# Performance work log

Measured on AMD Instinct MI355X. Metric: run time of the kernel, lower is better.

Reference implementation:

```python
import jax, jax.numpy as jnp
import numpy as np

# BQQ block dims: Y_sign (p,j,k,m,l), Z_sign (p,j,k,l,n); in=k*n=4096, out=j*m=4096
P, J, K, M, L, N = 2, 32, 32, 128, 16, 128
ACT_BITS = 8  # activation quantization bits


def setup_inputs() -> dict:
    key = jax.random.key(0)
    ks = jax.random.split(key, 7)
    x = jax.random.normal(ks[0], (1, 512, K * N), dtype=jnp.float32)
    # sign matrices in {-1,+1}
    Y_sign = jnp.where(jax.random.normal(ks[1], (P, J, K, M, L)) >= 0, 1.0, -1.0).astype(jnp.float32)
    Z_sign = jnp.where(jax.random.normal(ks[2], (P, J, K, L, N)) >= 0, 1.0, -1.0).astype(jnp.float32)
    # per-block positive scales (abs-mean in the original, so strictly > 0)
    Y_scale = jax.random.uniform(ks[3], (P, J, K, 1, 1), minval=0.01, maxval=0.1, dtype=jnp.float32)
    Z_scale = jax.random.uniform(ks[4], (P, J, K, 1, 1), minval=0.01, maxval=0.1, dtype=jnp.float32)
    A = jax.random.normal(ks[5], (P, J, K, 4), dtype=jnp.float32) * 0.1
    bias = jax.random.normal(ks[6], (J * M,), dtype=jnp.float32) * 0.1
    return {"input": x, "Y_sign": Y_sign, "Z_sign": Z_sign,
            "Y_scale": Y_scale, "Z_scale": Z_scale, "A": A, "bias": bias}


def reference(input, Y_sign, Z_sign, Y_scale, Z_scale, A, bias):
    # --- activation quantization (act_bits = 8, simple round, no STE) ---
    qmax = float(2 ** (ACT_BITS - 1) - 1)  # 127
    x_max = jnp.max(input)
    x_min = jnp.min(input)
    act_scale = jnp.maximum((x_max - x_min) / (2.0 * qmax), 1e-8)
    X = jnp.clip(jnp.round(input / act_scale), -qmax, qmax) * act_scale

    # --- dequantize sign * scale ---
    Y_q = Y_sign * Y_scale  # (p,j,k,m,l)
    Z_q = Z_sign * Z_scale  # (p,j,k,l,n)

    orig_shape = X.shape[:-1]
    X_kn = X.reshape(-1, K, N)  # (B,k,n)

    # chained block einsums
    T = jnp.einsum('bkn,pjkln->bpjkl', X_kn, Z_q)          # (B,p,j,k,l)
    core = jnp.einsum('pjkml,bpjkl->bpjkm', Y_q, T)        # (B,p,j,k,m)

    # quant_bias=True correction terms: A[...,0..3] = (a,b,c,d)
    out1 = jnp.einsum('bpjkm,pjk->bjm', core, A[..., 0])

    Y_sum = Y_q.sum(axis=-1)                               # (p,j,k,m)
    B_coef = jnp.einsum('pjk,pjkm->jkm', A[..., 1], Y_sum)
    Sx = X_kn.sum(axis=-1)                                 # (B,k)
    out2 = jnp.einsum('bk,jkm->bjm', Sx, B_coef)

    Zs = Z_q.sum(axis=-2)                                  # (p,j,k,n)
    Tz = jnp.einsum('bkn,pjkn->bpjk', X_kn, Zs)
    out3 = jnp.einsum('bpjk,pjk->bj', Tz, A[..., 2])

    D_coef = A[..., 3].sum(axis=0)                         # (j,k)
    out4 = jnp.einsum('bk,jk->bj', Sx, D_coef)

    out_bjm = out1 + out2 + (out3 + out4)[:, :, None]      # (B,j,m)
    out_2d = out_bjm.reshape(-1, J * M) + bias
    return out_2d.reshape(*orig_shape, J * M)
```

## Files before the change

### kernel.cpp

```cpp
#include <hip/hip_runtime.h>
#include <hip/hip_bf16.h>

typedef __attribute__((ext_vector_type(4))) float f32x4;
typedef __attribute__((ext_vector_type(8))) short bf16x8;
typedef __attribute__((ext_vector_type(4))) unsigned int u32x4;

#define GLOBAL_AS __attribute__((address_space(1)))
#define LDS_AS __attribute__((address_space(3)))

static __device__ __forceinline__ unsigned short f2bf(float f) {
  __hip_bfloat16 h = __float2bfloat16(f);
  return __builtin_bit_cast(unsigned short, h);
}
static __device__ __forceinline__ float bf2f(unsigned short u) {
  unsigned int v = ((unsigned int)u) << 16;
  return __builtin_bit_cast(float, v);
}
static __device__ __forceinline__ void load_lds16(const void* g, void* l) {
  __builtin_amdgcn_global_load_lds((GLOBAL_AS void*)g, (LDS_AS void*)l, 16, 0, 0);
}

__global__ __launch_bounds__(256) void k_minmax_part(const float* __restrict__ x,
                                                     float* __restrict__ part) {
  int tid = blockIdx.x * 256 + threadIdx.x;
  const float4* xv = (const float4*)x;
  float mn = 3.4e38f, mx = -3.4e38f;
#pragma unroll
  for (int rep = 0; rep < 8; ++rep) {
    float4 v = xv[tid + rep * 65536];
    mn = fminf(mn, fminf(fminf(v.x, v.y), fminf(v.z, v.w)));
    mx = fmaxf(mx, fmaxf(fmaxf(v.x, v.y), fmaxf(v.z, v.w)));
  }
#pragma unroll
  for (int o = 32; o > 0; o >>= 1) {
    mn = fminf(mn, __shfl_down(mn, o));
    mx = fmaxf(mx, __shfl_down(mx, o));
  }
  __shared__ float smn[4], smx[4];
  int lane = threadIdx.x & 63, w = threadIdx.x >> 6;
  if (lane == 0) { smn[w] = mn; smx[w] = mx; }
  __syncthreads();
  if (threadIdx.x == 0) {
    mn = fminf(fminf(smn[0], smn[1]), fminf(smn[2], smn[3]));
    mx = fmaxf(fmaxf(smx[0], smx[1]), fmaxf(smx[2], smx[3]));
    part[2 * blockIdx.x] = mn;
    part[2 * blockIdx.x + 1] = mx;
  }
}

__global__ __launch_bounds__(256) void k_fused(const float* __restrict__ x,
                                               const float* __restrict__ part,
                                               const float* __restrict__ Ysg,
                                               const float* __restrict__ Zsg,
                                               const float* __restrict__ Ysc,
                                               const float* __restrict__ Zsc,
                                               const float* __restrict__ Acoef,
                                               float* __restrict__ scl,
                                               unsigned short* __restrict__ xq,
                                               unsigned short* __restrict__ W) {
  const int t = threadIdx.x;
  if (blockIdx.x < 1024) {
    const int jk = blockIdx.x;
    __shared__ unsigned short Yb[2 * 128 * 24];
    __shared__ unsigned short Zb[128 * 36];
    __shared__ float B1p[2][128];
    __shared__ float C1[128];
    float cf0[2], cf2[2], cf4[2];
    float Dv;
    {
      float ys0 = Ysc[jk], zs0 = Zsc[jk], ys1 = Ysc[1024 + jk], zs1 = Zsc[1024 + jk];
      const float* A0p = Acoef + (size_t)jk * 4;
      const float* A1p = Acoef + (size_t)(1024 + jk) * 4;
      cf0[0] = A0p[0] * ys0 * zs0; cf0[1] = A1p[0] * ys1 * zs1;
      cf2[0] = A0p[1] * ys0;       cf2[1] = A1p[1] * ys1;
      cf4[0] = A0p[2] * zs0;       cf4[1] = A1p[2] * zs1;
      Dv = A0p[3] + A1p[3];
    }
#pragma unroll
    for (int rep = 0; rep < 4; ++rep) {
      int q = rep * 256 + t;
      int l0 = (q & 3) * 4, m = (q >> 2) & 127, p = q >> 9;
      float4 v = *(const float4*)(Ysg + (size_t)(p * 1024 + jk) * 2048 + m * 16 + l0);
      float s4 = v.x + v.y + v.z + v.w;
      s4 += __shfl_xor(s4, 1);
      s4 += __shfl_xor(s4, 2);
      if ((t & 3) == 0) B1p[p][m] = s4;
      float c0 = cf0[p];
      ushort4 o = make_ushort4(f2bf(c0 * v.x), f2bf(c0 * v.y), f2bf(c0 * v.z), f2bf(c0 * v.w));
      *(ushort4*)&Yb[(p * 128 + m) * 24 + l0] = o;
    }
#pragma unroll
    for (int rep = 0; rep < 4; ++rep) {
      int q = rep * 256 + t;
      int n0 = (q & 31) * 4, l = (q >> 5) & 15, p = q >> 9;
      float4 v = *(const float4*)(Zsg + (size_t)(p * 1024 + jk) * 2048 + l * 128 + n0);
      int pl = p * 16 + l;
      Zb[(n0 + 0) * 36 + pl] = f2bf(v.x);
      Zb[(n0 + 1) * 36 + pl] = f2bf(v.y);
      Zb[(n0 + 2) * 36 + pl] = f2bf(v.z);
      Zb[(n0 + 3) * 36 + pl] = f2bf(v.w);
    }
    __syncthreads();
    if (t < 128) {
      float s0 = 0.f, s1 = 0.f;
#pragma unroll
      for (int l = 0; l < 16; ++l) {
        s0 += bf2f(Zb[t * 36 + l]);
        s1 += bf2f(Zb[t * 36 + 16 + l]);
      }
      C1[t] = cf4[0] * s0 + cf4[1] * s1;
    }
    __syncthreads();
    const int lane = t & 63, wid = t >> 6;
    const int wm = wid >> 1, wn = wid & 1;
    const int grp = lane >> 4;
    bf16x8 af[4], bfr[4];
#pragma unroll
    for (int fm = 0; fm < 4; ++fm) {
      int m = wm * 64 + fm * 16 + (lane & 15);
      af[fm] = *(const bf16x8*)((const char*)Yb + ((grp >> 1) * 128 + m) * 48 + (grp & 1) * 16);
    }
#pragma unroll
    for (int fn = 0; fn < 4; ++fn) {
      int n = wn * 64 + fn * 16 + (lane & 15);
      const char* zp = (const char*)Zb + n * 72 + grp * 16;
      uint2 z0 = *(const uint2*)zp;
      uint2 z1 = *(const uint2*)(zp + 8);
      u32x4 zw; zw[0] = z0.x; zw[1] = z0.y; zw[2] = z1.x; zw[3] = z1.y;
      bfr[fn] = __builtin_bit_cast(bf16x8, zw);
    }
    f32x4 acc[4][4];
#pragma unroll
    for (int fm = 0; fm < 4; ++fm)
#pragma unroll
      for (int fn = 0; fn < 4; ++fn)
        acc[fm][fn] = __builtin_amdgcn_mfma_f32_16x16x32_bf16(af[fm], bfr[fn], (f32x4)(0.f), 0, 0, 0);
    const int j = jk >> 5, k = jk & 31;
    float c1v[4];
#pragma unroll
    for (int fn = 0; fn < 4; ++fn) c1v[fn] = C1[wn * 64 + fn * 16 + (lane & 15)];
#pragma unroll
    for (int fm = 0; fm < 4; ++fm) {
#pragma unroll
      for (int i = 0; i < 4; ++i) {
        int row = wm * 64 + fm * 16 + (grp)*4 + i;
        float b1v = cf2[0] * B1p[0][row] + cf2[1] * B1p[1][row] + Dv;
        size_t rowoff = (size_t)(j * 128 + row) * 4096 + (size_t)(k * 128);
#pragma unroll
        for (int fn = 0; fn < 4; ++fn) {
          int col = wn * 64 + fn * 16 + (lane & 15);
          W[rowoff + col] = f2bf(acc[fm][fn][i] + b1v + c1v[fn]);
        }
      }
    }
  } else {
    const int qb = blockIdx.x - 1024;
    float2 v2 = ((const float2*)part)[t];
    float mn = v2.x, mx = v2.y;
#pragma unroll
    for (int o = 32; o > 0; o >>= 1) {
      mn = fminf(mn, __shfl_down(mn, o));
      mx = fmaxf(mx, __shfl_down(mx, o));
    }
    __shared__ float smn2[4], smx2[4], ssc[1];
    int lane = t & 63, w = t >> 6;
    if (lane == 0) { smn2[w] = mn; smx2[w] = mx; }
    __syncthreads();
    if (t == 0) {
      mn = fminf(fminf(smn2[0], smn2[1]), fminf(smn2[2], smn2[3]));
      mx = fmaxf(fmaxf(smx2[0], smx2[1]), fmaxf(smx2[2], smx2[3]));
      ssc[0] = fmaxf((mx - mn) / 254.0f, 1e-8f);
      if (qb == 0) scl[0] = ssc[0];
    }
    __syncthreads();
    const float s = ssc[0];
    int i = qb * 256 + t;
    float4 v = ((const float4*)x)[i];
    float a = fminf(fmaxf(rintf(v.x / s), -127.f), 127.f);
    float b = fminf(fmaxf(rintf(v.y / s), -127.f), 127.f);
    float c = fminf(fmaxf(rintf(v.z / s), -127.f), 127.f);
    float d = fminf(fmaxf(rintf(v.w / s), -127.f), 127.f);
    ((ushort4*)xq)[i] = make_ushort4(f2bf(a), f2bf(b), f2bf(c), f2bf(d));
  }
}

__global__ __launch_bounds__(512) void k_gemm(const unsigned short* __restrict__ Xq,
                                              const unsigned short* __restrict__ W,
                                              unsigned short* __restrict__ P) {
  __shared__ unsigned short Al[2][256 * 64];
  __shared__ unsigned short Bl[2][256 * 64];
  const int t = threadIdx.x, lane = t & 63, wid = t >> 6;
  const int wg = (blockIdx.x & 7) * 32 + (blockIdx.x >> 3);
  const int sk = wg >> 5;
  const int bm = (wg >> 4) & 1;
  const int bn = wg & 15;
  const int wm = wid >> 2, wn = wid & 3;
  const int kbase = sk * 512;
  f32x4 acc[8][4];
#pragma unroll
  for (int a = 0; a < 8; ++a)
#pragma unroll
    for (int b = 0; b < 4; ++b) acc[a][b] = (f32x4)(0.f);

  const int lr = lane >> 3;
  const int lcb = (lane & 7) * 16;

  auto STAGE = [&](int buf, int kt) {
    const int k0 = kbase + kt * 64;
#pragma unroll
    for (int c = 0; c < 4; ++c) {
      int chunk = wid * 4 + c;
      int r = chunk * 8 + lr;
      int colb = lcb ^ ((r & 7) << 4);
      load_lds16(Xq + ((size_t)(bm * 256 + r) << 12) + k0 + (colb >> 1), &Al[buf][chunk * 512]);
    }
#pragma unroll
    for (int c = 0; c < 4; ++c) {
      int chunk = wid * 4 + c;
      int r = chunk * 8 + lr;
      int colb = lcb ^ ((r & 7) << 4);
      load_lds16(W + ((size_t)(bn * 256 + r) << 12) + k0 + (colb >> 1), &Bl[buf][chunk * 512]);
    }
  };

  auto COMPUTE = [&](int buf) {
#pragma unroll
    for (int ks = 0; ks < 2; ++ks) {
      bf16x8 af[8], bfr[4];
#pragma unroll
      for (int fm = 0; fm < 8; ++fm) {
        int r = wm * 128 + fm * 16 + (lane & 15);
        int colb = (ks * 64 + ((lane >> 4) * 16)) ^ ((r & 7) << 4);
        af[fm] = *(const bf16x8*)((const char*)&Al[buf][0] + r * 128 + colb);
      }
#pragma unroll
      for (int fn = 0; fn < 4; ++fn) {
        int r = wn * 64 + fn * 16 + (lane & 15);
        int colb = (ks * 64 + ((lane >> 4) * 16)) ^ ((r & 7) << 4);
        bfr[fn] = *(const bf16x8*)((const char*)&Bl[buf][0] + r * 128 + colb);
      }
#pragma unroll
      for (int fm = 0; fm < 8; ++fm)
#pragma unroll
        for (int fn = 0; fn < 4; ++fn)
          acc[fm][fn] = __builtin_amdgcn_mfma_f32_16x16x32_bf16(af[fm], bfr[fn], acc[fm][fn], 0, 0, 0);
    }
  };

  STAGE(0, 0);
  for (int it = 0; it < 8; ++it) {
    STAGE((it + 1) & 1, (it + 1) & 7);
    __builtin_amdgcn_sched_barrier(0);
    asm volatile("s_waitcnt vmcnt(8)" ::: "memory");
    __builtin_amdgcn_sched_barrier(0);
    __builtin_amdgcn_s_barrier();
    __builtin_amdgcn_sched_barrier(0);
    COMPUTE(it & 1);
    __builtin_amdgcn_sched_barrier(0);
    __builtin_amdgcn_s_barrier();
  }

  unsigned short* Pk = P + (size_t)sk * 2097152;
  const int blkL = bm * 16 + bn;
#pragma unroll
  for (int fm = 0; fm < 8; ++fm) {
#pragma unroll
    for (int fn = 0; fn < 4; ++fn) {
      int idx = (((blkL * 8 + wid) * 32 + fm * 4 + fn) * 64) + lane;
      ushort4 o = make_ushort4(f2bf(acc[fm][fn][0]), f2bf(acc[fm][fn][1]),
                               f2bf(acc[fm][fn][2]), f2bf(acc[fm][fn][3]));
      ((ushort4*)Pk)[idx] = o;
    }
  }
}

__global__ __launch_bounds__(256) void k_epi(float* __restrict__ out,
                                             const unsigned short* __restrict__ P,
                                             const float* __restrict__ scl,
                                             const float* __restrict__ bias) {
  int g = blockIdx.x * 256 + threadIdx.x;
  const int lane = g & 63;
  const int ff = (g >> 6) & 31;
  const int fn = ff & 3, fm = ff >> 2;
  const int wid = (g >> 11) & 7;
  const int blkL = g >> 14;
  const int bm = blkL >> 4, bn = blkL & 15;
  const int wm = wid >> 2, wn = wid & 3;
  const int row0 = bm * 256 + wm * 128 + fm * 16 + ((lane >> 4) << 2);
  const int col = bn * 256 + wn * 64 + fn * 16 + (lane & 15);
  const float s = scl[0];
  const float bv = bias[col];
  float sum[4] = {0.f, 0.f, 0.f, 0.f};
#pragma unroll
  for (int k = 0; k < 8; ++k) {
    ushort4 p = ((const ushort4*)(P + (size_t)k * 2097152))[g];
    sum[0] += bf2f(p.x); sum[1] += bf2f(p.y); sum[2] += bf2f(p.z); sum[3] += bf2f(p.w);
  }
#pragma unroll
  for (int i = 0; i < 4; ++i) out[(size_t)(row0 + i) * 4096 + col] = sum[i] * s + bv;
}

__global__ __launch_bounds__(512) void k_gemm_fb(const unsigned short* __restrict__ Xq,
                                                 const unsigned short* __restrict__ W,
                                                 const float* __restrict__ scl,
                                                 const float* __restrict__ bias,
                                                 float* __restrict__ out) {
  __shared__ unsigned short Al[4][128 * 64];
  __shared__ unsigned short Bl[4][64 * 64];
  const int t = threadIdx.x, lane = t & 63, wid = t >> 6;
  const int wg = (blockIdx.x & 7) * 32 + (blockIdx.x >> 3);
  const int bm = wg & 3;
  const int bn = wg >> 2;
  const int wm = wid >> 1, wn = wid & 1;
  f32x4 acc[2][2];
#pragma unroll
  for (int a = 0; a < 2; ++a)
#pragma unroll
    for (int b = 0; b < 2; ++b) acc[a][b] = (f32x4)(0.f);
  const int lr = lane >> 3;
  const int lcb = (lane & 7) * 16;
  auto STAGE = [&](int buf, int kt) {
    const int k0 = kt * 64;
#pragma unroll
    for (int c = 0; c < 2; ++c) {
      int chunk = wid * 2 + c;
      int r = chunk * 8 + lr;
      int colb = lcb ^ ((r & 7) << 4);
      load_lds16(Xq + ((size_t)(bm * 128 + r) << 12) + k0 + (colb >> 1), &Al[buf][chunk * 512]);
    }
    {
      int r = wid * 8 + lr;
      int colb = lcb ^ ((r & 7) << 4);
      load_lds16(W + ((size_t)(bn * 64 + r) << 12) + k0 + (colb >> 1), &Bl[buf][wid * 512]);
    }
  };
  auto COMPUTE = [&](int buf) {
#pragma unroll
    for (int ks = 0; ks < 2; ++ks) {
      bf16x8 af[2], bfr[2];
#pragma unroll
      for (int fm = 0; fm < 2; ++fm) {
        int r = wm * 32 + fm * 16 + (lane & 15);
        int colb = (ks * 64 + ((lane >> 4) * 16)) ^ ((r & 7) << 4);
        af[fm] = *(const bf16x8*)((const char*)&Al[buf][0] + r * 128 + colb);
      }
#pragma unroll
      for (int fn = 0; fn < 2; ++fn) {
        int r = wn * 32 + fn * 16 + (lane & 15);
        int colb = (ks * 64 + ((lane >> 4) * 16)) ^ ((r & 7) << 4);
        bfr[fn] = *(const bf16x8*)((const char*)&Bl[buf][0] + r * 128 + colb);
      }
#pragma unroll
      for (int fm = 0; fm < 2; ++fm)
#pragma unroll
        for (int fn = 0; fn < 2; ++fn)
          acc[fm][fn] = __builtin_amdgcn_mfma_f32_16x16x32_bf16(af[fm], bfr[fn], acc[fm][fn], 0, 0, 0);
    }
  };
  STAGE(0, 0); STAGE(1, 1); STAGE(2, 2);
  for (int t64 = 0; t64 < 64; ++t64) {
    STAGE((t64 + 3) & 3, (t64 + 3) & 63);
    __builtin_amdgcn_sched_barrier(0);
    asm volatile("s_waitcnt vmcnt(9)" ::: "memory");
    __builtin_amdgcn_sched_barrier(0);
    __builtin_amdgcn_s_barrier();
    __builtin_amdgcn_sched_barrier(0);
    COMPUTE(t64 & 3);
    __builtin_amdgcn_sched_barrier(0);
    __builtin_amdgcn_s_barrier();
  }
  const float s = scl[0];
#pragma unroll
  for (int fn = 0; fn < 2; ++fn) {
    int col = bn * 64 + wn * 32 + fn * 16 + (lane & 15);
    float bv = bias[col];
#pragma unroll
    for (int fm = 0; fm < 2; ++fm) {
#pragma unroll
      for (int i = 0; i < 4; ++i) {
        int row = bm * 128 + wm * 32 + fm * 16 + (lane >> 4) * 4 + i;
        out[(size_t)row * 4096 + col] = acc[fm][fn][i] * s + bv;
      }
    }
  }
}

extern "C" void kernel_launch(void* const* d_in, const int* in_sizes, int n_in,
                              void* d_out, int out_size, void* d_ws, size_t ws_size,
                              hipStream_t stream) {
  const float* x    = (const float*)d_in[0];
  const float* Ysg  = (const float*)d_in[1];
  const float* Zsg  = (const float*)d_in[2];
  const float* Ysc  = (const float*)d_in[3];
  const float* Zsc  = (const float*)d_in[4];
  const float* A    = (const float*)d_in[5];
  const float* bias = (const float*)d_in[6];
  float* out = (float*)d_out;

  char* ws = (char*)d_ws;
  float* scl  = (float*)ws;
  float* part = (float*)(ws + 256);
  unsigned short* Xq = (unsigned short*)(ws + 65536);
  unsigned short* W  = (unsigned short*)(ws + 65536 + (size_t)4194304);
  unsigned short* P  = (unsigned short*)(ws + 65536 + (size_t)4194304 + (size_t)33554432);

  k_minmax_part<<<dim3(256), dim3(256), 0, stream>>>(x, part);
  k_fused<<<dim3(3072), dim3(256), 0, stream>>>(x, part, Ysg, Zsg, Ysc, Zsc, A, scl, Xq, W);
  if (ws_size >= (size_t)65536 + 4194304 + 33554432 + 33554432) {
    k_gemm<<<dim3(256), dim3(512), 0, stream>>>(Xq, W, P);
    k_epi<<<dim3(2048), dim3(256), 0, stream>>>(out, P, scl, bias);
  } else {
    k_gemm_fb<<<dim3(256), dim3(512), 0, stream>>>(Xq, W, scl, bias, out);
  }
}
```

Measured before the change: 55.55 us.

## Deepen GEMM LDS pipeline to four stages with 32-wide K tiles

The GEMM kernel's LDS staging moves from two 64-wide K buffers to four 32-wide K buffers, with three stages prefetched ahead and a matching vmcnt wait. The XOR swizzle is replaced by a rotation swizzle suited to 64-byte rows. MFMA issue is wrapped in s_setprio to favour the math wave during compute. The aim is to hide global-load latency better at the same LDS footprint, at the cost of twice as many barrier pairs per K and smaller compute chunks between syncs.

```diff
diff --git a/kernel.cpp b/kernel.cpp
--- a/kernel.cpp
+++ b/kernel.cpp
@@ -187,8 +187,8 @@
 __global__ __launch_bounds__(512) void k_gemm(const unsigned short* __restrict__ Xq,
                                               const unsigned short* __restrict__ W,
                                               unsigned short* __restrict__ P) {
-  __shared__ unsigned short Al[2][256 * 64];
-  __shared__ unsigned short Bl[2][256 * 64];
+  __shared__ unsigned short Al[4][256 * 32];
+  __shared__ unsigned short Bl[4][256 * 32];
   const int t = threadIdx.x, lane = t & 63, wid = t >> 6;
   const int wg = (blockIdx.x & 7) * 32 + (blockIdx.x >> 3);
   const int sk = wg >> 5;
@@ -202,60 +202,59 @@
 #pragma unroll
     for (int b = 0; b < 4; ++b) acc[a][b] = (f32x4)(0.f);
 
-  const int lr = lane >> 3;
-  const int lcb = (lane & 7) * 16;
+  const int srow = lane >> 2;
+  const int sphys = lane & 3;
 
   auto STAGE = [&](int buf, int kt) {
-    const int k0 = kbase + kt * 64;
-#pragma unroll
-    for (int c = 0; c < 4; ++c) {
-      int chunk = wid * 4 + c;
-      int r = chunk * 8 + lr;
-      int colb = lcb ^ ((r & 7) << 4);
-      load_lds16(Xq + ((size_t)(bm * 256 + r) << 12) + k0 + (colb >> 1), &Al[buf][chunk * 512]);
-    }
-#pragma unroll
-    for (int c = 0; c < 4; ++c) {
-      int chunk = wid * 4 + c;
-      int r = chunk * 8 + lr;
-      int colb = lcb ^ ((r & 7) << 4);
-      load_lds16(W + ((size_t)(bn * 256 + r) << 12) + k0 + (colb >> 1), &Bl[buf][chunk * 512]);
+    const int k0 = kbase + kt * 32;
+#pragma unroll
+    for (int c2 = 0; c2 < 2; ++c2) {
+      int chunk = wid * 2 + c2;
+      int r = chunk * 16 + srow;
+      int g = (sphys - (r >> 1)) & 3;
+      load_lds16(Xq + ((size_t)(bm * 256 + r) << 12) + k0 + g * 8, &Al[buf][chunk * 512]);
+    }
+#pragma unroll
+    for (int c2 = 0; c2 < 2; ++c2) {
+      int chunk = wid * 2 + c2;
+      int r = chunk * 16 + srow;
+      int g = (sphys - (r >> 1)) & 3;
+      load_lds16(W + ((size_t)(bn * 256 + r) << 12) + k0 + g * 8, &Bl[buf][chunk * 512]);
     }
   };
 
-  auto COMPUTE = [&](int buf) {
-#pragma unroll
-    for (int ks = 0; ks < 2; ++ks) {
-      bf16x8 af[8], bfr[4];
-#pragma unroll
-      for (int fm = 0; fm < 8; ++fm) {
-        int r = wm * 128 + fm * 16 + (lane & 15);
-        int colb = (ks * 64 + ((lane >> 4) * 16)) ^ ((r & 7) << 4);
-        af[fm] = *(const bf16x8*)((const char*)&Al[buf][0] + r * 128 + colb);
-      }
-#pragma unroll
-      for (int fn = 0; fn < 4; ++fn) {
-        int r = wn * 64 + fn * 16 + (lane & 15);
-        int colb = (ks * 64 + ((lane >> 4) * 16)) ^ ((r & 7) << 4);
-        bfr[fn] = *(const bf16x8*)((const char*)&Bl[buf][0] + r * 128 + colb);
-      }
-#pragma unroll
-      for (int fm = 0; fm < 8; ++fm)
-#pragma unroll
-        for (int fn = 0; fn < 4; ++fn)
-          acc[fm][fn] = __builtin_amdgcn_mfma_f32_16x16x32_bf16(af[fm], bfr[fn], acc[fm][fn], 0, 0, 0);
-    }
-  };
-
   STAGE(0, 0);
-  for (int it = 0; it < 8; ++it) {
-    STAGE((it + 1) & 1, (it + 1) & 7);
-    __builtin_amdgcn_sched_barrier(0);
-    asm volatile("s_waitcnt vmcnt(8)" ::: "memory");
+  STAGE(1, 1);
+  STAGE(2, 2);
+  for (int it = 0; it < 16; ++it) {
+    STAGE((it + 3) & 3, (it + 3) & 15);
+    __builtin_amdgcn_sched_barrier(0);
+    asm volatile("s_waitcnt vmcnt(12)" ::: "memory");
     __builtin_amdgcn_sched_barrier(0);
     __builtin_amdgcn_s_barrier();
     __builtin_amdgcn_sched_barrier(0);
-    COMPUTE(it & 1);
+    const int cur = it & 3;
+    bf16x8 af[8], bfr[4];
+#pragma unroll
+    for (int fm = 0; fm < 8; ++fm) {
+      int r = wm * 128 + fm * 16 + (lane & 15);
+      int s = ((lane >> 4) + (r >> 1)) & 3;
+      af[fm] = *(const bf16x8*)((const char*)&Al[cur][0] + r * 64 + s * 16);
+    }
+#pragma unroll
+    for (int fn = 0; fn < 4; ++fn) {
+      int r = wn * 64 + fn * 16 + (lane & 15);
+      int s = ((lane >> 4) + (r >> 1)) & 3;
+      bfr[fn] = *(const bf16x8*)((const char*)&Bl[cur][0] + r * 64 + s * 16);
+    }
+    __builtin_amdgcn_sched_barrier(0);
+    __builtin_amdgcn_s_setprio(1);
+#pragma unroll
+    for (int fm = 0; fm < 8; ++fm)
+#pragma unroll
+      for (int fn = 0; fn < 4; ++fn)
+        acc[fm][fn] = __builtin_amdgcn_mfma_f32_16x16x32_bf16(af[fm], bfr[fn], acc[fm][fn], 0, 0, 0);
+    __builtin_amdgcn_s_setprio(0);
     __builtin_amdgcn_sched_barrier(0);
     __builtin_amdgcn_s_barrier();
   }
```

New measurement: 59.82 us. 1.08x slower.

## Interleave next-tile global-to-LDS loads with MFMA sub-phases in GEMM main loop

Applied to the files above, without the earlier changes.

Splits each K-tile's staging into four half-loads (A and B halves) and the compute into four sub-phases (two fm halves by two k-steps). Each sub-phase issues one slice of the next tile's loads before its MFMAs, so memory traffic overlaps the math instead of being issued all at once. It also raises wave priority around the MFMA bursts with s_setprio. The vmcnt wait changes to vmcnt(2) after the first slice, which relies on exact load-count accounting. This adds more LDS read phases and more scheduling barriers.

```diff
diff --git a/kernel.cpp b/kernel.cpp
--- a/kernel.cpp
+++ b/kernel.cpp
@@ -205,58 +205,73 @@
   const int lr = lane >> 3;
   const int lcb = (lane & 7) * 16;
 
-  auto STAGE = [&](int buf, int kt) {
+  auto STAGE_A2 = [&](int buf, int kt, int half) {
     const int k0 = kbase + kt * 64;
 #pragma unroll
-    for (int c = 0; c < 4; ++c) {
-      int chunk = wid * 4 + c;
+    for (int c = 0; c < 2; ++c) {
+      int chunk = wid * 4 + half * 2 + c;
       int r = chunk * 8 + lr;
       int colb = lcb ^ ((r & 7) << 4);
       load_lds16(Xq + ((size_t)(bm * 256 + r) << 12) + k0 + (colb >> 1), &Al[buf][chunk * 512]);
     }
-#pragma unroll
-    for (int c = 0; c < 4; ++c) {
-      int chunk = wid * 4 + c;
+  };
+  auto STAGE_B2 = [&](int buf, int kt, int half) {
+    const int k0 = kbase + kt * 64;
+#pragma unroll
+    for (int c = 0; c < 2; ++c) {
+      int chunk = wid * 4 + half * 2 + c;
       int r = chunk * 8 + lr;
       int colb = lcb ^ ((r & 7) << 4);
       load_lds16(W + ((size_t)(bn * 256 + r) << 12) + k0 + (colb >> 1), &Bl[buf][chunk * 512]);
     }
   };
 
-  auto COMPUTE = [&](int buf) {
-#pragma unroll
-    for (int ks = 0; ks < 2; ++ks) {
-      bf16x8 af[8], bfr[4];
-#pragma unroll
-      for (int fm = 0; fm < 8; ++fm) {
+  STAGE_A2(0, 0, 0); STAGE_A2(0, 0, 1);
+  STAGE_B2(0, 0, 0); STAGE_B2(0, 0, 1);
+
+  for (int it = 0; it < 8; ++it) {
+    const int cur = it & 1, nxt = cur ^ 1;
+    const int ktn = (it + 1) & 7;
+#pragma unroll
+    for (int sp = 0; sp < 4; ++sp) {
+      if (sp == 0)      STAGE_A2(nxt, ktn, 0);
+      else if (sp == 1) STAGE_A2(nxt, ktn, 1);
+      else if (sp == 2) STAGE_B2(nxt, ktn, 0);
+      else              STAGE_B2(nxt, ktn, 1);
+      if (sp == 0) {
+        __builtin_amdgcn_sched_barrier(0);
+        asm volatile("s_waitcnt vmcnt(2)" ::: "memory");
+        __builtin_amdgcn_sched_barrier(0);
+        __builtin_amdgcn_s_barrier();
+        __builtin_amdgcn_sched_barrier(0);
+      }
+      const int fmh = sp & 1;
+      const int ksh = sp >> 1;
+      bf16x8 af[4], bfr[4];
+#pragma unroll
+      for (int f = 0; f < 4; ++f) {
+        int fm = fmh * 4 + f;
         int r = wm * 128 + fm * 16 + (lane & 15);
-        int colb = (ks * 64 + ((lane >> 4) * 16)) ^ ((r & 7) << 4);
-        af[fm] = *(const bf16x8*)((const char*)&Al[buf][0] + r * 128 + colb);
+        int colb = (ksh * 64 + ((lane >> 4) * 16)) ^ ((r & 7) << 4);
+        af[f] = *(const bf16x8*)((const char*)&Al[cur][0] + r * 128 + colb);
       }
 #pragma unroll
       for (int fn = 0; fn < 4; ++fn) {
         int r = wn * 64 + fn * 16 + (lane & 15);
-        int colb = (ks * 64 + ((lane >> 4) * 16)) ^ ((r & 7) << 4);
-        bfr[fn] = *(const bf16x8*)((const char*)&Bl[buf][0] + r * 128 + colb);
-      }
-#pragma unroll
-      for (int fm = 0; fm < 8; ++fm)
+        int colb = (ksh * 64 + ((lane >> 4) * 16)) ^ ((r & 7) << 4);
+        bfr[fn] = *(const bf16x8*)((const char*)&Bl[cur][0] + r * 128 + colb);
+      }
+      __builtin_amdgcn_sched_barrier(0);
+      __builtin_amdgcn_s_setprio(1);
+#pragma unroll
+      for (int f = 0; f < 4; ++f)
 #pragma unroll
         for (int fn = 0; fn < 4; ++fn)
-          acc[fm][fn] = __builtin_amdgcn_mfma_f32_16x16x32_bf16(af[fm], bfr[fn], acc[fm][fn], 0, 0, 0);
-    }
-  };
-
-  STAGE(0, 0);
-  for (int it = 0; it < 8; ++it) {
-    STAGE((it + 1) & 1, (it + 1) & 7);
-    __builtin_amdgcn_sched_barrier(0);
-    asm volatile("s_waitcnt vmcnt(8)" ::: "memory");
-    __builtin_amdgcn_sched_barrier(0);
-    __builtin_amdgcn_s_barrier();
-    __builtin_amdgcn_sched_barrier(0);
-    COMPUTE(it & 1);
-    __builtin_amdgcn_sched_barrier(0);
+          acc[fmh * 4 + f][fn] =
+              __builtin_amdgcn_mfma_f32_16x16x32_bf16(af[f], bfr[fn], acc[fmh * 4 + f][fn], 0, 0, 0);
+      __builtin_amdgcn_s_setprio(0);
+      __builtin_amdgcn_sched_barrier(0);
+    }
     __builtin_amdgcn_s_barrier();
   }
 
```

Result: slower. 57.97 us (+4.3%).
